# Performance work log

Measured on AMD Instinct MI355X. Metric: run time of the kernel, lower is better.

Reference implementation:

```python
import jax, jax.numpy as jnp
import numpy as np

L, B, H, R = 128, 4, 768, 97
LN_EPS = 1e-5


def setup_inputs() -> dict:
    key = jax.random.key(0)
    ks = jax.random.split(key, 8)
    s = 0.02
    return {
        "h_re1": jax.random.normal(ks[0], (L, B, H), jnp.float32),
        "h_re2": jax.random.normal(ks[1], (L, B, H), jnp.float32),
        "mask": jax.random.uniform(ks[2], (L, B), jnp.float32),
        "Wr": jax.random.normal(ks[3], (H, 2 * H), jnp.float32) * s,
        "br": jnp.zeros((H,), jnp.float32),
        "Wh": jax.random.normal(ks[4], (H, 3 * H), jnp.float32) * s,
        "bh": jnp.zeros((H,), jnp.float32),
        "gamma": jnp.ones((H,), jnp.float32),
        "beta": jnp.zeros((H,), jnp.float32),
        "Wo": jax.random.normal(ks[5], (R, H), jnp.float32) * s,
        "bo": jnp.zeros((R,), jnp.float32),
    }


def reference(h_re1, h_re2, mask, Wr, br, Wh, bh, gamma, beta, Wo, bo):
    # h_re1, h_re2: [L, B, H]; mask: [L, B]
    h = h_re2.shape[-1]
    # global context: tanh(Linear(cat(h_re1,h_re2))), max over length -> [B, H]
    g = jnp.tanh(jnp.einsum('lbi,hi->lbh', jnp.concatenate([h_re1, h_re2], axis=-1), Wr) + br)
    g = jnp.max(g, axis=0)  # [B, H]
    # hid2hid(cat(r1, r2, g)) == r1 @ W1.T + r2 @ W2.T + g @ W3.T + b
    # (avoids materializing the [L,L,B,3H] repeat+cat tensor)
    W1, W2, W3 = Wh[:, :h], Wh[:, h:2 * h], Wh[:, 2 * h:]
    a = jnp.einsum('lbi,hi->lbh', h_re2, W1)          # varies over first pair axis
    b2 = jnp.einsum('lbi,hi->lbh', h_re2, W2)         # varies over second pair axis
    gp = jnp.einsum('bi,hi->bh', g, W3) + bh          # constant over pairs
    pre = a[:, None, :, :] + b2[None, :, :, :] + gp   # [L, L, B, H]
    # LayerNorm over last dim (biased variance, as in torch)
    mu = jnp.mean(pre, axis=-1, keepdims=True)
    var = jnp.var(pre, axis=-1, keepdims=True)
    x = (pre - mu) * jax.lax.rsqrt(var + LN_EPS) * gamma + beta
    x = jax.nn.elu(x)  # dropout is identity in eval mode
    out = jax.nn.sigmoid(jnp.einsum('klbh,rh->klbr', x, Wo) + bo)  # [L, L, B, R]
    # pairwise mask: mask_e1 * mask_e2, broadcast over relation dim
    m = mask[:, None, :, None] * mask[None, :, :, None]
    return out * m
```

## Files before the change

kernel.cpp:

```cpp
#include <hip/hip_runtime.h>
#include <hip/hip_bf16.h>
#include <stdint.h>

#define L_ 128
#define B_ 4
#define H_ 768
#define R_ 97
#define LN_EPS 1e-5f

typedef _Float16 f16x8 __attribute__((ext_vector_type(8)));
typedef _Float16 f16x4 __attribute__((ext_vector_type(4)));
typedef _Float16 f16x2 __attribute__((ext_vector_type(2)));
typedef float f32x4 __attribute__((ext_vector_type(4)));

extern "C" __device__ _Float16 __ocml_exp2_f16(_Float16);

__global__ __launch_bounds__(256) void prep_all(const float* __restrict__ h1,
                                                const float* __restrict__ h2,
                                                const float* __restrict__ Wr,
                                                const float* __restrict__ Wh,
                                                const float* __restrict__ Wo,
                                                const float* __restrict__ gamma,
                                                const float* __restrict__ beta,
                                                _Float16* __restrict__ ccH,
                                                _Float16* __restrict__ Bp,
                                                _Float16* __restrict__ WoP,
                                                _Float16* __restrict__ gbH,
                                                unsigned int* __restrict__ gmaxU) {
  int blk = blockIdx.x;
  if (blk < 512) {
    const float2* s1 = (const float2*)(h1 + (size_t)blk * H_);
    const float2* s2 = (const float2*)(h2 + (size_t)blk * H_);
    f16x2* d = (f16x2*)(ccH + (size_t)blk * (2 * H_));
    for (int i = threadIdx.x; i < H_ / 2; i += 256) {
      float2 v = s1[i]; f16x2 o; o[0] = (_Float16)v.x; o[1] = (_Float16)v.y; d[i] = o;
    }
    for (int i = threadIdx.x; i < H_ / 2; i += 256) {
      float2 v = s2[i]; f16x2 o; o[0] = (_Float16)v.x; o[1] = (_Float16)v.y; d[H_ / 2 + i] = o;
    }
    return;
  }
  blk -= 512;
  if (blk < 6912) {
    int f = (blk * 256 + threadIdx.x) * 2;
    int j = f & 7;
    int u = f >> 3;
    int lidx = u & 63; u >>= 6;
    int nt = u % 144;
    int ks = u / 144;
    int k = ks * 32 + (lidx >> 4) * 8 + j;
    int n = nt * 16 + (lidx & 15);
    float v0, v1;
    if (n < 768) {
      v0 = Wr[(size_t)n * 1536 + k];
      v1 = Wr[(size_t)n * 1536 + k + 1];
    } else if (n < 1536) {
      int n2 = n - 768;
      if (k >= 768) { v0 = Wh[(size_t)n2 * 2304 + (k - 768)]; v1 = Wh[(size_t)n2 * 2304 + (k - 767)]; }
      else { v0 = 0.f; v1 = 0.f; }
    } else {
      int n2 = n - 1536;
      if (k >= 768) { v0 = Wh[(size_t)n2 * 2304 + 768 + (k - 768)]; v1 = Wh[(size_t)n2 * 2304 + 768 + (k - 767)]; }
      else { v0 = 0.f; v1 = 0.f; }
    }
    f16x2 o; o[0] = (_Float16)v0; o[1] = (_Float16)v1;
    *(f16x2*)(Bp + f) = o;
    return;
  }
  blk -= 6912;
  if (blk < 192) {
    int f = (blk * 256 + threadIdx.x) * 2;
    int j = f & 7;
    int u = f >> 3;
    int lidx = u & 63; u >>= 6;
    int nt = u & 7;
    int ks = u >> 3;
    int k = ks * 32 + (lidx >> 4) * 8 + j;
    int n = nt * 16 + (lidx & 15);
    float v0 = 0.f, v1 = 0.f;
    if (n < R_) { v0 = Wo[(size_t)n * H_ + k]; v1 = Wo[(size_t)n * H_ + k + 1]; }
    f16x2 o; o[0] = (_Float16)v0; o[1] = (_Float16)v1;
    *(f16x2*)(WoP + f) = o;
    return;
  }
  blk -= 192;
  if (blk < 3) {
    int i = blk * 256 + threadIdx.x;
    if (i < H_) {
      gbH[i] = (_Float16)gamma[i];
      gbH[H_ + i] = (_Float16)beta[i];
    }
    return;
  }
  blk -= 3;
  int i = blk * 256 + threadIdx.x;
  if (i < B_ * H_) gmaxU[i] = 0u;
}

__global__ __launch_bounds__(256) void gemm_big(const _Float16* __restrict__ A,
                                                const _Float16* __restrict__ Bp,
                                                const float* __restrict__ br,
                                                unsigned int* __restrict__ gmaxU,
                                                _Float16* __restrict__ aH,
                                                _Float16* __restrict__ bH) {
  int w = threadIdx.x >> 6, l = threadIdx.x & 63;
  int nb = blockIdx.x, mb = blockIdx.y;
  int row0 = mb * 32 + (w & 1) * 16;
  int nt0 = nb * 4 + (w >> 1) * 2;
  const f16x8* ap = (const f16x8*)(A + (size_t)(row0 + (l & 15)) * 1536 + (l >> 4) * 8);
  const f16x8* bp = (const f16x8*)(Bp + ((size_t)nt0 * 64 + l) * 8);
  f32x4 acc0 = {}, acc1 = {};
  f16x8 ac = ap[0], b0c = bp[0], b1c = bp[64];
  for (int ks = 0; ks < 48; ++ks) {
    f16x8 an = {}, b0n = {}, b1n = {};
    if (ks < 47) {
      an = ap[(ks + 1) * 4];
      b0n = bp[(size_t)(ks + 1) * 9216];
      b1n = bp[(size_t)(ks + 1) * 9216 + 64];
    }
    acc0 = __builtin_amdgcn_mfma_f32_16x16x32_f16(ac, b0c, acc0, 0, 0, 0);
    acc1 = __builtin_amdgcn_mfma_f32_16x16x32_f16(ac, b1c, acc1, 0, 0, 0);
    ac = an; b0c = b0n; b1c = b1n;
  }
#pragma unroll
  for (int q = 0; q < 2; ++q) {
    f32x4 acc = q ? acc1 : acc0;
    int col = nb * 64 + (w >> 1) * 32 + q * 16 + (l & 15);
#pragma unroll
    for (int r = 0; r < 4; ++r) {
      int row = row0 + (l >> 4) * 4 + r;
      float v = acc[r];
      if (col < 768) {
        float t = tanhf(v + br[col]) + 1.0f;
        atomicMax(&gmaxU[(row & 3) * H_ + col], __float_as_uint(t));
      } else if (col < 1536) {
        aH[(size_t)row * H_ + (col - 768)] = (_Float16)v;
      } else {
        bH[(size_t)row * H_ + (col - 1536)] = (_Float16)v;
      }
    }
  }
}

__global__ __launch_bounds__(256) void gp_kernel(const float* __restrict__ Wh,
                                                 const unsigned int* __restrict__ gmaxU,
                                                 const float* __restrict__ bh,
                                                 float* __restrict__ gpv) {
  int n = blockIdx.x;
  int w = threadIdx.x >> 6, l = threadIdx.x & 63;
  const float* wr = Wh + (size_t)n * 2304 + 1536;
  const unsigned int* gm = gmaxU + (size_t)w * H_;
  float s = 0.f;
#pragma unroll
  for (int t = 0; t < 12; ++t) {
    int i = l + 64 * t;
    s += wr[i] * (__uint_as_float(gm[i]) - 1.0f);
  }
#pragma unroll
  for (int off = 32; off; off >>= 1) s += __shfl_xor(s, off);
  if (l == 0) gpv[(size_t)w * H_ + n] = s + bh[n];
}

__global__ __launch_bounds__(256) void stats(const _Float16* __restrict__ aH,
                                             const _Float16* __restrict__ bH,
                                             const float* __restrict__ gpv,
                                             _Float16* __restrict__ aH2,
                                             float* __restrict__ S,
                                             float* __restrict__ Q) {
  int r = blockIdx.x * 4 + (threadIdx.x >> 6);
  int l = threadIdx.x & 63;
  float s = 0.f, q = 0.f;
  if (r < 512) {
    int b = r & 3;
    const f16x4* ap = (const f16x4*)(aH + (size_t)r * H_);
    const float4* gp4 = (const float4*)(gpv + (size_t)b * H_);
    f16x4* op = (f16x4*)(aH2 + (size_t)r * H_);
#pragma unroll
    for (int t = 0; t < 3; ++t) {
      int i = t * 64 + l;
      f16x4 av = ap[i];
      float4 g4 = gp4[i];
      f16x4 o;
      o[0] = (_Float16)((float)av[0] + g4.x);
      o[1] = (_Float16)((float)av[1] + g4.y);
      o[2] = (_Float16)((float)av[2] + g4.z);
      o[3] = (_Float16)((float)av[3] + g4.w);
      op[i] = o;
#pragma unroll
      for (int j = 0; j < 4; ++j) { float y = (float)o[j]; s += y; q += y * y; }
    }
  } else {
    const f16x4* bp = (const f16x4*)(bH + (size_t)(r - 512) * H_);
#pragma unroll
    for (int t = 0; t < 3; ++t) {
      f16x4 bv = bp[t * 64 + l];
#pragma unroll
      for (int j = 0; j < 4; ++j) { float y = (float)bv[j]; s += y; q += y * y; }
    }
  }
#pragma unroll
  for (int off = 32; off; off >>= 1) {
    s += __shfl_xor(s, off);
    q += __shfl_xor(q, off);
  }
  if (l == 0) { S[r] = s; Q[r] = q; }
}

__global__ __launch_bounds__(256) void dotab(const _Float16* __restrict__ aH2,
                                             const _Float16* __restrict__ bH,
                                             const float* __restrict__ S,
                                             const float* __restrict__ Q,
                                             float* __restrict__ mu_arr,
                                             float* __restrict__ rs_arr) {
  int w = threadIdx.x >> 6, l = threadIdx.x & 63;
  int ltq = blockIdx.x, kt = blockIdx.y, b = blockIdx.z;
  int lt = ltq * 4 + w;
  const f16x8* ap = (const f16x8*)(aH2 + ((size_t)(kt * 16 + (l & 15)) * 4 + b) * H_ + (l >> 4) * 8);
  const f16x8* bp = (const f16x8*)(bH + ((size_t)(lt * 16 + (l & 15)) * 4 + b) * H_ + (l >> 4) * 8);
  f32x4 acc = {};
  f16x8 a0 = ap[0], b0 = bp[0], a1 = ap[4], b1 = bp[4];
  for (int ks = 0; ks < 24; ++ks) {
    f16x8 a2 = {}, b2 = {};
    if (ks < 22) { a2 = ap[(ks + 2) * 4]; b2 = bp[(ks + 2) * 4]; }
    acc = __builtin_amdgcn_mfma_f32_16x16x32_f16(a0, b0, acc, 0, 0, 0);
    a0 = a1; b0 = b1; a1 = a2; b1 = b2;
  }
#pragma unroll
  for (int r = 0; r < 4; ++r) {
    int k = kt * 16 + (l >> 4) * 4 + r;
    int lg = lt * 16 + (l & 15);
    int arow = k * 4 + b, brow = lg * 4 + b;
    float mu = (S[arow] + S[512 + brow]) * (1.f / H_);
    float q2 = Q[arow] + Q[512 + brow] + 2.f * acc[r];
    float var = fmaxf(q2 * (1.f / H_) - mu * mu, 0.f);
    float rs = rsqrtf(var + LN_EPS);
    size_t idx = (size_t)k * 512 + (size_t)lg * 4 + b;
    mu_arr[idx] = mu;
    rs_arr[idx] = rs;
  }
}

__global__ __launch_bounds__(256) void fused2(const _Float16* __restrict__ aH2,
                                              const _Float16* __restrict__ bH,
                                              const _Float16* __restrict__ gbH,
                                              const _Float16* __restrict__ WoP,
                                              const float* __restrict__ bo,
                                              const float* __restrict__ mask,
                                              const float* __restrict__ mu_arr,
                                              const float* __restrict__ rs_arr,
                                              float* __restrict__ out) {
  __shared__ __align__(16) _Float16 WoLds[2][4096];
  int tid = threadIdx.x, w = tid >> 6, l = tid & 63;
  int m0 = blockIdx.x * 64;
  int myrow = m0 + w * 16 + (l & 15);
  int b = myrow & 3, li = (myrow >> 2) & 127, kk = myrow >> 9;
  const f16x8* ap = (const f16x8*)(aH2 + ((size_t)kk * 4 + b) * H_ + (l >> 4) * 8);
  const f16x8* bp = (const f16x8*)(bH + ((size_t)li * 4 + b) * H_ + (l >> 4) * 8);
  const f16x8* gp8 = (const f16x8*)(gbH + (l >> 4) * 8);
  const f16x8* be8 = (const f16x8*)(gbH + H_ + (l >> 4) * 8);
  float mu = mu_arr[myrow], rs = rs_arr[myrow];
  _Float16 muh = (_Float16)mu, rsh = (_Float16)rs;
  _Float16 l2e = (_Float16)1.44269504f;
  f16x8 mu8, rs8, zero8, one8, l2e8;
#pragma unroll
  for (int j = 0; j < 8; ++j) {
    mu8[j] = muh; rs8[j] = rsh;
    zero8[j] = (_Float16)0.f; one8[j] = (_Float16)1.f; l2e8[j] = l2e;
  }

  const uint4* wog = (const uint4*)WoP;
  uint4* lds0 = (uint4*)&WoLds[0][0];
  lds0[tid] = wog[tid];
  lds0[256 + tid] = wog[256 + tid];
  __syncthreads();

  f16x8 a8 = ap[0], b8 = bp[0], g8 = gp8[0], e8 = be8[0];

  f32x4 acc[7] = {};
  for (int ks = 0; ks < 24; ++ks) {
    int cur = ks & 1;
    uint4 wo0 = {}, wo1 = {};
    f16x8 an = {}, bn = {}, gn = {}, en = {};
    if (ks < 23) {
      wo0 = wog[(ks + 1) * 512 + tid];
      wo1 = wog[(ks + 1) * 512 + 256 + tid];
      an = ap[(ks + 1) * 4];
      bn = bp[(ks + 1) * 4];
      gn = gp8[(ks + 1) * 4];
      en = be8[(ks + 1) * 4];
    }
    f16x8 x = a8 + b8;
    f16x8 c1 = rs8 * g8;
    f16x8 yv = (x - mu8) * c1 + e8;
    f16x8 y2 = yv * l2e8;
    f16x8 ex;
#pragma unroll
    for (int j = 0; j < 8; ++j) ex[j] = __ocml_exp2_f16(y2[j]);
    ex = ex - one8;
    f16x8 av = __builtin_elementwise_max(yv, zero8) + __builtin_elementwise_min(ex, zero8);
    __syncthreads();
    if (ks < 23) {
      uint4* d = (uint4*)&WoLds[cur ^ 1][0];
      d[tid] = wo0;
      d[256 + tid] = wo1;
    }
    __syncthreads();
    const f16x8* bvp = (const f16x8*)&WoLds[cur][0];
#pragma unroll
    for (int q = 0; q < 7; ++q) {
      f16x8 bv = bvp[q * 64 + l];
      acc[q] = __builtin_amdgcn_mfma_f32_16x16x32_f16(av, bv, acc[q], 0, 0, 0);
    }
    a8 = an; b8 = bn; g8 = gn; e8 = en;
  }
  float mv[4];
#pragma unroll
  for (int r = 0; r < 4; ++r) {
    int row = m0 + w * 16 + (l >> 4) * 4 + r;
    int bb = row & 3, ll = (row >> 2) & 127, kx = row >> 9;
    mv[r] = mask[kx * 4 + bb] * mask[ll * 4 + bb];
  }
#pragma unroll
  for (int q = 0; q < 7; ++q) {
    int col = q * 16 + (l & 15);
    if (col < R_) {
      float bov = bo[col];
#pragma unroll
      for (int r = 0; r < 4; ++r) {
        int row = m0 + w * 16 + (l >> 4) * 4 + r;
        float z = acc[q][r] + bov;
        out[(size_t)row * R_ + col] = mv[r] / (1.f + __expf(-z));
      }
    }
  }
}

extern "C" void kernel_launch(void* const* d_in, const int* in_sizes, int n_in,
                              void* d_out, int out_size, void* d_ws, size_t ws_size,
                              hipStream_t stream) {
  const float* h1    = (const float*)d_in[0];
  const float* h2    = (const float*)d_in[1];
  const float* mask  = (const float*)d_in[2];
  const float* Wr    = (const float*)d_in[3];
  const float* br    = (const float*)d_in[4];
  const float* Wh    = (const float*)d_in[5];
  const float* bh    = (const float*)d_in[6];
  const float* gamma = (const float*)d_in[7];
  const float* beta  = (const float*)d_in[8];
  const float* Wo    = (const float*)d_in[9];
  const float* bo    = (const float*)d_in[10];
  float* out = (float*)d_out;
  char* ws = (char*)d_ws;

  _Float16* ccH = (_Float16*)ws;                    size_t off = 512 * 1536 * 2;
  _Float16* Bp  = (_Float16*)(ws + off);            off += (size_t)1536 * 2304 * 2;
  _Float16* WoP = (_Float16*)(ws + off);            off += 768 * 128 * 2;
  _Float16* gbH = (_Float16*)(ws + off);            off += 4096;
  _Float16* aH  = (_Float16*)(ws + off);            off += 512 * 768 * 2;
  _Float16* bH  = (_Float16*)(ws + off);            off += 512 * 768 * 2;
  _Float16* aH2 = (_Float16*)(ws + off);            off += 512 * 768 * 2;
  unsigned int* gmaxU = (unsigned int*)(ws + off);  off += 3072 * 4;
  float* gpv = (float*)(ws + off);                  off += 3072 * 4;
  float* S   = (float*)(ws + off);                  off += 1024 * 4;
  float* Q   = (float*)(ws + off);                  off += 1024 * 4;
  float* mu_arr = (float*)(ws + off);               off += 65536 * 4;
  float* rs_arr = (float*)(ws + off);               off += 65536 * 4;

  prep_all<<<512 + 6912 + 192 + 3 + 12, 256, 0, stream>>>(h1, h2, Wr, Wh, Wo, gamma, beta,
                                                          ccH, Bp, WoP, gbH, gmaxU);

  gemm_big<<<dim3(36, 16), 256, 0, stream>>>(ccH, Bp, br, gmaxU, aH, bH);
  gp_kernel<<<768, 256, 0, stream>>>(Wh, gmaxU, bh, gpv);
  stats<<<256, 256, 0, stream>>>(aH, bH, gpv, aH2, S, Q);
  dotab<<<dim3(2, 8, 4), 256, 0, stream>>>(aH2, bH, S, Q, mu_arr, rs_arr);

  fused2<<<1024, 256, 0, stream>>>(aH2, bH, gbH, WoP, bo, mask, mu_arr, rs_arr, out);
}
```

Measured before the change: 100.4 us.

## Split fused projection GEMM to skip zero-padded K half and vectorize weight packing

The single combined GEMM used a K=1536 packed weight where the hid2hid columns had zeros for the first half of K. It is now split into two GEMMs: one for the global-context tanh/max over the full K, and one for the a/b projections over only the h_re2 half (K=768). This removes the multiply-by-zero MFMA work and shrinks the packed weight buffer. The weight repacking in prep_all also moves from 2-element scalar loads to float4 loads with 8-wide half stores, which lowers the prep block count. The cost is one extra kernel launch and less parallelism per launch.

```diff
diff --git a/kernel.cpp b/kernel.cpp
--- a/kernel.cpp
+++ b/kernel.cpp
@@ -14,6 +14,13 @@
 typedef float f32x4 __attribute__((ext_vector_type(4)));
 
 extern "C" __device__ _Float16 __ocml_exp2_f16(_Float16);
+
+__device__ inline f16x8 cvt8(float4 v0, float4 v1) {
+  f16x8 o;
+  o[0] = (_Float16)v0.x; o[1] = (_Float16)v0.y; o[2] = (_Float16)v0.z; o[3] = (_Float16)v0.w;
+  o[4] = (_Float16)v1.x; o[5] = (_Float16)v1.y; o[6] = (_Float16)v1.z; o[7] = (_Float16)v1.w;
+  return o;
+}
 
 __global__ __launch_bounds__(256) void prep_all(const float* __restrict__ h1,
                                                 const float* __restrict__ h2,
@@ -23,7 +30,8 @@
                                                 const float* __restrict__ gamma,
                                                 const float* __restrict__ beta,
                                                 _Float16* __restrict__ ccH,
-                                                _Float16* __restrict__ Bp,
+                                                _Float16* __restrict__ BpR,
+                                                _Float16* __restrict__ BpW,
                                                 _Float16* __restrict__ WoP,
                                                 _Float16* __restrict__ gbH,
                                                 unsigned int* __restrict__ gmaxU) {
@@ -41,49 +49,45 @@
     return;
   }
   blk -= 512;
-  if (blk < 6912) {
-    int f = (blk * 256 + threadIdx.x) * 2;
-    int j = f & 7;
-    int u = f >> 3;
-    int lidx = u & 63; u >>= 6;
-    int nt = u % 144;
-    int ks = u / 144;
-    int k = ks * 32 + (lidx >> 4) * 8 + j;
-    int n = nt * 16 + (lidx & 15);
-    float v0, v1;
-    if (n < 768) {
-      v0 = Wr[(size_t)n * 1536 + k];
-      v1 = Wr[(size_t)n * 1536 + k + 1];
-    } else if (n < 1536) {
-      int n2 = n - 768;
-      if (k >= 768) { v0 = Wh[(size_t)n2 * 2304 + (k - 768)]; v1 = Wh[(size_t)n2 * 2304 + (k - 767)]; }
-      else { v0 = 0.f; v1 = 0.f; }
-    } else {
-      int n2 = n - 1536;
-      if (k >= 768) { v0 = Wh[(size_t)n2 * 2304 + 768 + (k - 768)]; v1 = Wh[(size_t)n2 * 2304 + 768 + (k - 767)]; }
-      else { v0 = 0.f; v1 = 0.f; }
-    }
-    f16x2 o; o[0] = (_Float16)v0; o[1] = (_Float16)v1;
-    *(f16x2*)(Bp + f) = o;
+  if (blk < 576) {
+    int c = blk * 256 + threadIdx.x;
+    int l = c & 63, u = c >> 6;
+    int nt = u % 48, ks = u / 48;
+    int n = nt * 16 + (l & 15);
+    int k = ks * 32 + ((l >> 4) << 3);
+    const float4* s = (const float4*)(Wr + (size_t)n * 1536 + k);
+    *(f16x8*)(BpR + (size_t)c * 8) = cvt8(s[0], s[1]);
     return;
   }
-  blk -= 6912;
-  if (blk < 192) {
-    int f = (blk * 256 + threadIdx.x) * 2;
-    int j = f & 7;
-    int u = f >> 3;
-    int lidx = u & 63; u >>= 6;
-    int nt = u & 7;
-    int ks = u >> 3;
-    int k = ks * 32 + (lidx >> 4) * 8 + j;
-    int n = nt * 16 + (lidx & 15);
-    float v0 = 0.f, v1 = 0.f;
-    if (n < R_) { v0 = Wo[(size_t)n * H_ + k]; v1 = Wo[(size_t)n * H_ + k + 1]; }
-    f16x2 o; o[0] = (_Float16)v0; o[1] = (_Float16)v1;
-    *(f16x2*)(WoP + f) = o;
+  blk -= 576;
+  if (blk < 576) {
+    int c = blk * 256 + threadIdx.x;
+    int l = c & 63, u = c >> 6;
+    int nt = u % 96, ks = u / 96;
+    int n = nt * 16 + (l & 15);
+    int k = ks * 32 + ((l >> 4) << 3);
+    const float* src = (n < 768) ? (Wh + (size_t)n * 2304 + k)
+                                 : (Wh + (size_t)(n - 768) * 2304 + 768 + k);
+    const float4* s = (const float4*)src;
+    *(f16x8*)(BpW + (size_t)c * 8) = cvt8(s[0], s[1]);
     return;
   }
-  blk -= 192;
+  blk -= 576;
+  if (blk < 48) {
+    int c = blk * 256 + threadIdx.x;
+    int l = c & 63, u = c >> 6;
+    int nt = u & 7, ks = u >> 3;
+    int n = nt * 16 + (l & 15);
+    int k = ks * 32 + ((l >> 4) << 3);
+    f16x8 o = {};
+    if (n < R_) {
+      const float4* s = (const float4*)(Wo + (size_t)n * 768 + k);
+      o = cvt8(s[0], s[1]);
+    }
+    *(f16x8*)(WoP + (size_t)c * 8) = o;
+    return;
+  }
+  blk -= 48;
   if (blk < 3) {
     int i = blk * 256 + threadIdx.x;
     if (i < H_) {
@@ -97,26 +101,24 @@
   if (i < B_ * H_) gmaxU[i] = 0u;
 }
 
-__global__ __launch_bounds__(256) void gemm_big(const _Float16* __restrict__ A,
-                                                const _Float16* __restrict__ Bp,
-                                                const float* __restrict__ br,
-                                                unsigned int* __restrict__ gmaxU,
-                                                _Float16* __restrict__ aH,
-                                                _Float16* __restrict__ bH) {
+__global__ __launch_bounds__(256) void gemm_g(const _Float16* __restrict__ A,
+                                              const _Float16* __restrict__ BpR,
+                                              const float* __restrict__ br,
+                                              unsigned int* __restrict__ gmaxU) {
   int w = threadIdx.x >> 6, l = threadIdx.x & 63;
   int nb = blockIdx.x, mb = blockIdx.y;
   int row0 = mb * 32 + (w & 1) * 16;
   int nt0 = nb * 4 + (w >> 1) * 2;
   const f16x8* ap = (const f16x8*)(A + (size_t)(row0 + (l & 15)) * 1536 + (l >> 4) * 8);
-  const f16x8* bp = (const f16x8*)(Bp + ((size_t)nt0 * 64 + l) * 8);
+  const f16x8* bp = (const f16x8*)(BpR + ((size_t)nt0 * 64 + l) * 8);
   f32x4 acc0 = {}, acc1 = {};
   f16x8 ac = ap[0], b0c = bp[0], b1c = bp[64];
   for (int ks = 0; ks < 48; ++ks) {
     f16x8 an = {}, b0n = {}, b1n = {};
     if (ks < 47) {
       an = ap[(ks + 1) * 4];
-      b0n = bp[(size_t)(ks + 1) * 9216];
-      b1n = bp[(size_t)(ks + 1) * 9216 + 64];
+      b0n = bp[(size_t)(ks + 1) * 3072];
+      b1n = bp[(size_t)(ks + 1) * 3072 + 64];
     }
     acc0 = __builtin_amdgcn_mfma_f32_16x16x32_f16(ac, b0c, acc0, 0, 0, 0);
     acc1 = __builtin_amdgcn_mfma_f32_16x16x32_f16(ac, b1c, acc1, 0, 0, 0);
@@ -129,15 +131,45 @@
 #pragma unroll
     for (int r = 0; r < 4; ++r) {
       int row = row0 + (l >> 4) * 4 + r;
+      float t = tanhf(acc[r] + br[col]) + 1.0f;
+      atomicMax(&gmaxU[(row & 3) * H_ + col], __float_as_uint(t));
+    }
+  }
+}
+
+__global__ __launch_bounds__(256) void gemm_ab(const _Float16* __restrict__ ccH,
+                                               const _Float16* __restrict__ BpW,
+                                               _Float16* __restrict__ aH,
+                                               _Float16* __restrict__ bH) {
+  int w = threadIdx.x >> 6, l = threadIdx.x & 63;
+  int nb = blockIdx.x, mb = blockIdx.y;
+  int row0 = mb * 32 + (w & 1) * 16;
+  int nt0 = nb * 4 + (w >> 1) * 2;
+  const f16x8* ap = (const f16x8*)(ccH + (size_t)(row0 + (l & 15)) * 1536 + 768 + (l >> 4) * 8);
+  const f16x8* bp = (const f16x8*)(BpW + ((size_t)nt0 * 64 + l) * 8);
+  f32x4 acc0 = {}, acc1 = {};
+  f16x8 ac = ap[0], b0c = bp[0], b1c = bp[64];
+  for (int ks = 0; ks < 24; ++ks) {
+    f16x8 an = {}, b0n = {}, b1n = {};
+    if (ks < 23) {
+      an = ap[(ks + 1) * 4];
+      b0n = bp[(size_t)(ks + 1) * 6144];
+      b1n = bp[(size_t)(ks + 1) * 6144 + 64];
+    }
+    acc0 = __builtin_amdgcn_mfma_f32_16x16x32_f16(ac, b0c, acc0, 0, 0, 0);
+    acc1 = __builtin_amdgcn_mfma_f32_16x16x32_f16(ac, b1c, acc1, 0, 0, 0);
+    ac = an; b0c = b0n; b1c = b1n;
+  }
+#pragma unroll
+  for (int q = 0; q < 2; ++q) {
+    f32x4 acc = q ? acc1 : acc0;
+    int col = nb * 64 + (w >> 1) * 32 + q * 16 + (l & 15);
+#pragma unroll
+    for (int r = 0; r < 4; ++r) {
+      int row = row0 + (l >> 4) * 4 + r;
       float v = acc[r];
-      if (col < 768) {
-        float t = tanhf(v + br[col]) + 1.0f;
-        atomicMax(&gmaxU[(row & 3) * H_ + col], __float_as_uint(t));
-      } else if (col < 1536) {
-        aH[(size_t)row * H_ + (col - 768)] = (_Float16)v;
-      } else {
-        bH[(size_t)row * H_ + (col - 1536)] = (_Float16)v;
-      }
+      if (col < 768) aH[(size_t)row * H_ + col] = (_Float16)v;
+      else           bH[(size_t)row * H_ + (col - 768)] = (_Float16)v;
     }
   }
 }
@@ -353,7 +385,8 @@
   char* ws = (char*)d_ws;
 
   _Float16* ccH = (_Float16*)ws;                    size_t off = 512 * 1536 * 2;
-  _Float16* Bp  = (_Float16*)(ws + off);            off += (size_t)1536 * 2304 * 2;
+  _Float16* BpR = (_Float16*)(ws + off);            off += (size_t)1536 * 768 * 2;
+  _Float16* BpW = (_Float16*)(ws + off);            off += (size_t)768 * 1536 * 2;
   _Float16* WoP = (_Float16*)(ws + off);            off += 768 * 128 * 2;
   _Float16* gbH = (_Float16*)(ws + off);            off += 4096;
   _Float16* aH  = (_Float16*)(ws + off);            off += 512 * 768 * 2;
@@ -366,10 +399,11 @@
   float* mu_arr = (float*)(ws + off);               off += 65536 * 4;
   float* rs_arr = (float*)(ws + off);               off += 65536 * 4;
 
-  prep_all<<<512 + 6912 + 192 + 3 + 12, 256, 0, stream>>>(h1, h2, Wr, Wh, Wo, gamma, beta,
-                                                          ccH, Bp, WoP, gbH, gmaxU);
-
-  gemm_big<<<dim3(36, 16), 256, 0, stream>>>(ccH, Bp, br, gmaxU, aH, bH);
+  prep_all<<<512 + 576 + 576 + 48 + 3 + 12, 256, 0, stream>>>(h1, h2, Wr, Wh, Wo, gamma, beta,
+                                                              ccH, BpR, BpW, WoP, gbH, gmaxU);
+
+  gemm_g<<<dim3(12, 16), 256, 0, stream>>>(ccH, BpR, br, gmaxU);
+  gemm_ab<<<dim3(24, 16), 256, 0, stream>>>(ccH, BpW, aH, bH);
   gp_kernel<<<768, 256, 0, stream>>>(Wh, gmaxU, bh, gpv);
   stats<<<256, 256, 0, stream>>>(aH, bH, gpv, aH2, S, Q);
   dotab<<<dim3(2, 8, 4), 256, 0, stream>>>(aH2, bH, S, Q, mu_arr, rs_arr);
```

Result: slower. 102.8 us (+2.4%).
